# Kernel tuning notes

Hardware: AMD Instinct MI355X
Metric: run time of the kernel (lower is better)

## Reference

```python
import jax, jax.numpy as jnp
import numpy as np

B, S, D = 8, 2048, 128

def setup_inputs() -> dict:
    key = jax.random.key(0)
    kq, kk, kv, km = jax.random.split(key, 4)
    q = jax.random.normal(kq, (B, S, D), dtype=jnp.float32)
    k = jax.random.normal(kk, (B, S, D), dtype=jnp.float32)
    v = jax.random.normal(kv, (B, S, D), dtype=jnp.float32)
    mask = jax.random.randint(km, (B, S), 0, 2).astype(bool)  # True = masked out
    return {"q": q, "k": k, "v": v, "mask": mask}

def reference(q, k, v, mask):
    scaler = np.sqrt(D).astype(np.float32)
    # score[b, i, j] = <q_i, k_j> / sqrt(d_k)
    score = jnp.einsum('bik,bjk->bij', q, k) / scaler
    score = score - jnp.max(score, axis=-1, keepdims=True)
    e = jnp.exp(score)
    # mask is (B, S_kv): broadcast across query positions, zero out masked keys
    e = jnp.where(mask[:, None, :], 0.0, e)
    a = e / jnp.sum(e, axis=-1, keepdims=True)
    c = jnp.einsum('bij,bjd->bid', a, v)
    return c
```

## Files before the change

kernel.cpp:

```cpp
#include <hip/hip_runtime.h>
#include <hip/hip_fp16.h>
#include <math.h>

typedef __attribute__((ext_vector_type(8))) short short8;
typedef __attribute__((ext_vector_type(16))) float floatx16;
typedef __attribute__((ext_vector_type(2))) __bf16 bf16x2;

namespace {
constexpr int Bn = 8;
constexpr int Sn = 2048;
constexpr int Dn = 128;
constexpr int BQ = 128;
constexpr int BK = 64;
constexpr int QTILES = Sn / BQ;
constexpr int NKB = Sn / BK;
constexpr int ROWS = Bn * Sn;
constexpr int NSPLIT = 4;
constexpr float SC2 = 0.12753102063642597f;
constexpr int TILE_USH = BK * Dn;
}

#if __has_builtin(__builtin_amdgcn_exp2f)
#define EXP2(x) __builtin_amdgcn_exp2f(x)
#else
#define EXP2(x) exp2f(x)
#endif

__device__ __forceinline__ unsigned short f2bf(float x) {
  union { float f; unsigned u; } a; a.f = x;
  unsigned r = a.u + 0x7fffu + ((a.u >> 16) & 1u);
  return (unsigned short)(r >> 16);
}

__device__ __forceinline__ unsigned pack2bf(float x, float y) {
  union { bf16x2 b; unsigned u; } c;
  c.b[0] = (__bf16)x; c.b[1] = (__bf16)y;
  return c.u;
}

__device__ __forceinline__ void gl_lds16(const void* g, void* l, int lane) {
#if __has_builtin(__builtin_amdgcn_global_load_lds)
  (void)lane;
  __builtin_amdgcn_global_load_lds((const __attribute__((address_space(1))) unsigned int*)g,
                                   (__attribute__((address_space(3))) unsigned int*)l, 16, 0, 0);
#else
  *(float4*)((char*)l + lane * 16) = *(const float4*)g;
#endif
}

__global__ __launch_bounds__(256)
void prep(const float* __restrict__ kg, const float* __restrict__ vg,
          const unsigned char* __restrict__ mraw,
          unsigned short* __restrict__ Kpg, unsigned short* __restrict__ Vpg,
          float* __restrict__ mb2g) {
  __shared__ __align__(16) float Vf[16 * 136];
  const int p = blockIdx.x;
  const int b = p >> 7, q = p & 127;
  const int kb = q >> 2, k16 = q & 3;
  const int t = threadIdx.x;

  unsigned wv = ((const unsigned int*)mraw)[t];
  int any1  = __syncthreads_or((wv & 0x0000ff00u) ? 1 : 0);
  int any23 = __syncthreads_or((wv & 0xffff0000u) ? 1 : 0);
  const int mlayout = any1 ? 1 : (any23 ? 2 : 0);
  if (p < 64) {
    int idx = p * 256 + t;
    bool ms;
    if (mlayout == 1)      ms = mraw[idx] != 0;
    else if (mlayout == 2) ms = ((const float*)mraw)[idx] != 0.0f;
    else                   ms = ((const int*)mraw)[idx] != 0;
    mb2g[idx] = ms ? -1e30f : 0.0f;
  }

  const int j  = t >> 4;
  const int o8 = t & 15;
  const size_t base = ((size_t)(b * Sn + kb * 64 + k16 * 16 + j)) * 32 + o8 * 2;
  const float4* k4 = (const float4*)kg;
  const float4* v4 = (const float4*)vg;

  {
    float4 a = k4[base], bq = k4[base + 1];
    union { unsigned u[4]; short8 s8; } pk;
    pk.u[0] = pack2bf(a.x, a.y);   pk.u[1] = pack2bf(a.z, a.w);
    pk.u[2] = pack2bf(bq.x, bq.y); pk.u[3] = pack2bf(bq.z, bq.w);
    const int jl = k16 * 16 + j;
    *(short8*)(Kpg + (size_t)(b * NKB + kb) * TILE_USH + jl * 128 + ((o8 ^ (jl & 7)) * 8)) = pk.s8;
  }
  {
    float4 a = v4[base], bq = v4[base + 1];
    *(float4*)&Vf[j * 136 + o8 * 8]     = a;
    *(float4*)&Vf[j * 136 + o8 * 8 + 4] = bq;
  }
  __syncthreads();
  {
    const int d = t >> 1, h = t & 1;
    union { unsigned u[4]; short8 s8; } pv;
    #pragma unroll
    for (int i = 0; i < 4; ++i)
      pv.u[i] = pack2bf(Vf[(h * 8 + 2 * i) * 136 + d], Vf[(h * 8 + 2 * i + 1) * 136 + d]);
    const int og = k16 * 2 + h;
    *(short8*)(Vpg + (size_t)(b * NKB + kb) * TILE_USH + d * 64 + ((og ^ (d & 7)) * 8)) = pv.s8;
  }
}

template<int SPLIT, bool DIRECT>
__global__ __launch_bounds__(256, 2)
void attn_fwd(const float* __restrict__ qg,
              const unsigned short* __restrict__ Kpg,
              const unsigned short* __restrict__ Vpg,
              const float* __restrict__ mb2g,
              float* __restrict__ outg, __half* __restrict__ Op,
              float* __restrict__ Mp, float* __restrict__ Lp) {
  __shared__ __align__(16) unsigned short Khi[2][TILE_USH];
  __shared__ __align__(16) unsigned short Vt[2][TILE_USH];
  __shared__ __align__(16) unsigned short Pq[4 * 2048];

  const int tid = threadIdx.x;
  const int bid = blockIdx.x;
  const int b   = bid & 7;
  const int q0  = ((bid >> 3) & (QTILES - 1)) * BQ;
  const int s   = bid >> 7;
  const int kb0 = s * (NKB / SPLIT);
  const int kbN = kb0 + NKB / SPLIT;
  const int w   = tid >> 6;
  const int L   = tid & 63;
  const int q   = L & 31;
  const int h   = L >> 5;
  const int sw  = q & 7;

  const char* ktile = (const char*)(Kpg + (size_t)b * NKB * TILE_USH);
  const char* vtile = (const char*)(Vpg + (size_t)b * NKB * TILE_USH);
  const int stagebase = w * 4096;

  short8 qh[8], ql[8];
  {
    const float* qrow = qg + (size_t)(b * Sn + q0 + w * 32 + q) * Dn;
    #pragma unroll
    for (int kstep = 0; kstep < 8; ++kstep) {
      float4 f0 = *(const float4*)(qrow + kstep * 16 + h * 8);
      float4 f1 = *(const float4*)(qrow + kstep * 16 + h * 8 + 4);
      float xs[8] = {f0.x, f0.y, f0.z, f0.w, f1.x, f1.y, f1.z, f1.w};
      #pragma unroll
      for (int j = 0; j < 8; ++j) {
        unsigned short hi = f2bf(xs[j]);
        union { unsigned u; float f; } hv; hv.u = ((unsigned)hi) << 16;
        qh[kstep][j] = (short)hi;
        ql[kstep][j] = (short)f2bf(xs[j] - hv.f);
      }
    }
  }

  float m_i = -INFINITY, l_i = 0.0f;
  floatx16 O32[4];
  #pragma unroll
  for (int dg = 0; dg < 4; ++dg)
    #pragma unroll
    for (int r = 0; r < 16; ++r) O32[dg][r] = 0.0f;

  unsigned short* pwave = Pq + w * 2048;

  {
    const char* kt = ktile + (size_t)kb0 * (TILE_USH * 2);
    const char* vt = vtile + (size_t)kb0 * (TILE_USH * 2);
    #pragma unroll
    for (int i = 0; i < 4; ++i) {
      const int off = stagebase + i * 1024;
      gl_lds16(kt + off + L * 16, (char*)Khi[0] + off, L);
      gl_lds16(vt + off + L * 16, (char*)Vt[0] + off, L);
    }
  }

  for (int kb = kb0; kb < kbN; ++kb) {
    const int cur = (kb - kb0) & 1;
    __syncthreads();

    if (kb + 1 < kbN) {
      const char* kt = ktile + (size_t)(kb + 1) * (TILE_USH * 2);
      const char* vt = vtile + (size_t)(kb + 1) * (TILE_USH * 2);
      #pragma unroll
      for (int i = 0; i < 4; ++i) {
        const int off = stagebase + i * 1024;
        gl_lds16(kt + off + L * 16, (char*)Khi[cur ^ 1] + off, L);
        gl_lds16(vt + off + L * 16, (char*)Vt[cur ^ 1] + off, L);
      }
    }

    const unsigned short* Kc = Khi[cur];
    const unsigned short* Vc = Vt[cur];

    const float4* mb4 = (const float4*)(mb2g + b * Sn + kb * BK);
    float4 mbv[2][4];
    #pragma unroll
    for (int kg = 0; kg < 2; ++kg)
      #pragma unroll
      for (int ro = 0; ro < 4; ++ro) mbv[kg][ro] = mb4[kg * 8 + ro * 2 + h];

    floatx16 a32[2];
    #pragma unroll
    for (int kg = 0; kg < 2; ++kg)
      #pragma unroll
      for (int r = 0; r < 16; ++r) a32[kg][r] = 0.0f;
    #pragma unroll
    for (int kstep = 0; kstep < 8; ++kstep) {
      const int ko = ((kstep * 2 + h) ^ sw) * 8;
      #pragma unroll
      for (int kg = 0; kg < 2; ++kg) {
        short8 kf = *(const short8*)&Kc[(kg * 32 + q) * 128 + ko];
        a32[kg] = __builtin_amdgcn_mfma_f32_32x32x16_bf16(kf, qh[kstep], a32[kg], 0, 0, 0);
        a32[kg] = __builtin_amdgcn_mfma_f32_32x32x16_bf16(kf, ql[kstep], a32[kg], 0, 0, 0);
      }
    }

    #pragma unroll
    for (int kg = 0; kg < 2; ++kg)
      #pragma unroll
      for (int ro = 0; ro < 4; ++ro) {
        float4 f = mbv[kg][ro];
        a32[kg][4 * ro + 0] = fmaf(a32[kg][4 * ro + 0], SC2, f.x);
        a32[kg][4 * ro + 1] = fmaf(a32[kg][4 * ro + 1], SC2, f.y);
        a32[kg][4 * ro + 2] = fmaf(a32[kg][4 * ro + 2], SC2, f.z);
        a32[kg][4 * ro + 3] = fmaf(a32[kg][4 * ro + 3], SC2, f.w);
      }
    float mx = -INFINITY;
    #pragma unroll
    for (int kg = 0; kg < 2; ++kg)
      #pragma unroll
      for (int r = 0; r < 16; ++r) mx = fmaxf(mx, a32[kg][r]);
    mx = fmaxf(mx, __shfl_xor(mx, 32));
    const float mnew = fmaxf(m_i, mx);
    const float alpha = EXP2(m_i - mnew);
    float rs = 0.0f;
    #pragma unroll
    for (int kg = 0; kg < 2; ++kg)
      #pragma unroll
      for (int r = 0; r < 16; ++r) {
        float e = EXP2(a32[kg][r] - mnew);
        a32[kg][r] = e;
        rs += e;
      }
    rs += __shfl_xor(rs, 32);
    l_i = l_i * alpha + rs;
    m_i = mnew;

    #pragma unroll
    for (int kg = 0; kg < 2; ++kg)
      #pragma unroll
      for (int ro = 0; ro < 4; ++ro) {
        uint2 u;
        u.x = pack2bf(a32[kg][4 * ro + 0], a32[kg][4 * ro + 1]);
        u.y = pack2bf(a32[kg][4 * ro + 2], a32[kg][4 * ro + 3]);
        const int oct = kg * 4 + ro;
        *(uint2*)&pwave[q * 64 + ((oct ^ sw) * 8) + h * 4] = u;
      }

    if (!__all(alpha == 1.0f)) {
      #pragma unroll
      for (int dg = 0; dg < 4; ++dg)
        #pragma unroll
        for (int r = 0; r < 16; ++r) O32[dg][r] *= alpha;
    }

    #pragma unroll
    for (int k2 = 0; k2 < 4; ++k2) {
      const int ko = ((k2 * 2 + h) ^ sw) * 8;
      short8 pf = *(const short8*)&pwave[q * 64 + ko];
      #pragma unroll
      for (int dg = 0; dg < 4; ++dg) {
        short8 vf = *(const short8*)&Vc[(dg * 32 + q) * 64 + ko];
        O32[dg] = __builtin_amdgcn_mfma_f32_32x32x16_bf16(vf, pf, O32[dg], 0, 0, 0);
      }
    }
  }

  const int row = b * Sn + q0 + w * 32 + q;
  if constexpr (DIRECT) {
    const float inv = 1.0f / l_i;
    float* orow = outg + (size_t)row * Dn;
    #pragma unroll
    for (int dg = 0; dg < 4; ++dg)
      #pragma unroll
      for (int ro = 0; ro < 4; ++ro) {
        float4 f = make_float4(O32[dg][4 * ro] * inv,     O32[dg][4 * ro + 1] * inv,
                               O32[dg][4 * ro + 2] * inv, O32[dg][4 * ro + 3] * inv);
        *(float4*)&orow[dg * 32 + 8 * ro + 4 * h] = f;
      }
  } else {
    __half* orow = Op + ((size_t)s * ROWS + row) * Dn;
    #pragma unroll
    for (int dg = 0; dg < 4; ++dg)
      #pragma unroll
      for (int ro = 0; ro < 4; ++ro) {
        union { __half2 h2[2]; uint2 u; } pk;
        pk.h2[0] = __floats2half2_rn(O32[dg][4 * ro],     O32[dg][4 * ro + 1]);
        pk.h2[1] = __floats2half2_rn(O32[dg][4 * ro + 2], O32[dg][4 * ro + 3]);
        *(uint2*)&orow[dg * 32 + 8 * ro + 4 * h] = pk.u;
      }
    if (h == 0) {
      Mp[s * ROWS + row] = m_i;
      Lp[s * ROWS + row] = l_i;
    }
  }
}

__global__ __launch_bounds__(256)
void attn_combine(const __half* __restrict__ Op, const float* __restrict__ Mp,
                  const float* __restrict__ Lp, float4* __restrict__ out4) {
  const int gid = blockIdx.x * 256 + threadIdx.x;
  const int row = gid >> 5;
  const int c4  = gid & 31;
  float ms[NSPLIT];
  float m = -INFINITY;
  #pragma unroll
  for (int s = 0; s < NSPLIT; ++s) { ms[s] = Mp[s * ROWS + row]; m = fmaxf(m, ms[s]); }
  float l = 0.0f;
  float4 acc = make_float4(0.f, 0.f, 0.f, 0.f);
  #pragma unroll
  for (int s = 0; s < NSPLIT; ++s) {
    float wgt = EXP2(ms[s] - m);
    l = fmaf(Lp[s * ROWS + row], wgt, l);
    union { uint2 u; __half2 h2[2]; } pk;
    pk.u = ((const uint2*)Op)[(size_t)(s * ROWS + row) * 32 + c4];
    float2 f0 = __half22float2(pk.h2[0]);
    float2 f1 = __half22float2(pk.h2[1]);
    acc.x = fmaf(f0.x, wgt, acc.x);
    acc.y = fmaf(f0.y, wgt, acc.y);
    acc.z = fmaf(f1.x, wgt, acc.z);
    acc.w = fmaf(f1.y, wgt, acc.w);
  }
  float inv = 1.0f / l;
  out4[(size_t)row * 32 + c4] = make_float4(acc.x * inv, acc.y * inv, acc.z * inv, acc.w * inv);
}

extern "C" void kernel_launch(void* const* d_in, const int* in_sizes, int n_in,
                              void* d_out, int out_size, void* d_ws, size_t ws_size,
                              hipStream_t stream) {
  const float* q = (const float*)d_in[0];
  const float* k = (const float*)d_in[1];
  const float* v = (const float*)d_in[2];
  const unsigned char* m = (const unsigned char*)d_in[3];
  float* out = (float*)d_out;
  (void)in_sizes; (void)n_in; (void)out_size;

  constexpr size_t OPB = (size_t)NSPLIT * ROWS * Dn * sizeof(__half);
  constexpr size_t MLB = (size_t)NSPLIT * ROWS * sizeof(float);
  constexpr size_t KPB = (size_t)Bn * NKB * TILE_USH * 2;
  constexpr size_t MBB = (size_t)ROWS * sizeof(float);

  char* ws = (char*)d_ws;
  if (ws_size >= OPB + 2 * MLB + 2 * KPB + MBB) {
    __half* Op = (__half*)ws;
    float* Mp = (float*)(ws + OPB);
    float* Lp = (float*)(ws + OPB + MLB);
    unsigned short* Kp = (unsigned short*)(ws + OPB + 2 * MLB);
    unsigned short* Vp = (unsigned short*)(ws + OPB + 2 * MLB + KPB);
    float* mb2 = (float*)(ws + OPB + 2 * MLB + 2 * KPB);
    prep<<<dim3(Bn * NKB * 4), dim3(256), 0, stream>>>(k, v, m, Kp, Vp, mb2);
    attn_fwd<NSPLIT, false><<<dim3(Bn * QTILES * NSPLIT), dim3(256), 0, stream>>>(
        q, Kp, Vp, mb2, out, Op, Mp, Lp);
    attn_combine<<<dim3(ROWS * 32 / 256), dim3(256), 0, stream>>>(
        Op, Mp, Lp, (float4*)out);
  } else if (ws_size >= 2 * KPB + MBB) {
    unsigned short* Kp = (unsigned short*)ws;
    unsigned short* Vp = (unsigned short*)(ws + KPB);
    float* mb2 = (float*)(ws + 2 * KPB);
    prep<<<dim3(Bn * NKB * 4), dim3(256), 0, stream>>>(k, v, m, Kp, Vp, mb2);
    attn_fwd<1, true><<<dim3(Bn * QTILES), dim3(256), 0, stream>>>(
        q, Kp, Vp, mb2, out, nullptr, nullptr, nullptr);
  }
}
```

Baseline: 114.5 us.

## Keep P in registers via permlane swap, defer rescaling, prioritize MFMA

Removes the per-wave LDS round trip for the softmax probability tile. The packed bf16 P values are rearranged between lane halves with permlane32_swap, so the PV MFMA takes its operand straight from registers. Online-softmax rescaling of O and l is skipped unless the block max exceeds the running max by more than a threshold, with a final correction using the true max. The change also adds s_setprio around the MFMA sections and splits the max and sum reductions into multiple accumulators for ILP. The risk is fp16 overflow of unnormalized partial outputs when rescaling is deferred, and extra register pressure.

```diff
diff --git a/kernel.cpp b/kernel.cpp
--- a/kernel.cpp
+++ b/kernel.cpp
@@ -5,6 +5,7 @@
 typedef __attribute__((ext_vector_type(8))) short short8;
 typedef __attribute__((ext_vector_type(16))) float floatx16;
 typedef __attribute__((ext_vector_type(2))) __bf16 bf16x2;
+typedef __attribute__((ext_vector_type(2))) unsigned int uint2v;
 
 namespace {
 constexpr int Bn = 8;
@@ -17,6 +18,7 @@
 constexpr int ROWS = Bn * Sn;
 constexpr int NSPLIT = 4;
 constexpr float SC2 = 0.12753102063642597f;
+constexpr float DEFER_THR = 8.0f;
 constexpr int TILE_USH = BK * Dn;
 }
 
@@ -36,6 +38,20 @@
   union { bf16x2 b; unsigned u; } c;
   c.b[0] = (__bf16)x; c.b[1] = (__bf16)y;
   return c.u;
+}
+
+__device__ __forceinline__ uint2v pl32swap(unsigned a, unsigned b, int h) {
+#if __has_builtin(__builtin_amdgcn_permlane32_swap)
+  (void)h;
+  return __builtin_amdgcn_permlane32_swap(a, b, false, false);
+#else
+  unsigned ax = __shfl_xor((int)a, 32);
+  unsigned bx = __shfl_xor((int)b, 32);
+  uint2v r;
+  r[0] = h ? bx : a;
+  r[1] = h ? b : ax;
+  return r;
+#endif
 }
 
 __device__ __forceinline__ void gl_lds16(const void* g, void* l, int lane) {
@@ -113,7 +129,6 @@
               float* __restrict__ Mp, float* __restrict__ Lp) {
   __shared__ __align__(16) unsigned short Khi[2][TILE_USH];
   __shared__ __align__(16) unsigned short Vt[2][TILE_USH];
-  __shared__ __align__(16) unsigned short Pq[4 * 2048];
 
   const int tid = threadIdx.x;
   const int bid = blockIdx.x;
@@ -151,13 +166,12 @@
   }
 
   float m_i = -INFINITY, l_i = 0.0f;
+  float mtrue = -INFINITY;
   floatx16 O32[4];
   #pragma unroll
   for (int dg = 0; dg < 4; ++dg)
     #pragma unroll
     for (int r = 0; r < 16; ++r) O32[dg][r] = 0.0f;
-
-  unsigned short* pwave = Pq + w * 2048;
 
   {
     const char* kt = ktile + (size_t)kb0 * (TILE_USH * 2);
@@ -200,6 +214,7 @@
     for (int kg = 0; kg < 2; ++kg)
       #pragma unroll
       for (int r = 0; r < 16; ++r) a32[kg][r] = 0.0f;
+    __builtin_amdgcn_s_setprio(1);
     #pragma unroll
     for (int kstep = 0; kstep < 8; ++kstep) {
       const int ko = ((kstep * 2 + h) ^ sw) * 8;
@@ -210,6 +225,7 @@
         a32[kg] = __builtin_amdgcn_mfma_f32_32x32x16_bf16(kf, ql[kstep], a32[kg], 0, 0, 0);
       }
     }
+    __builtin_amdgcn_s_setprio(0);
 
     #pragma unroll
     for (int kg = 0; kg < 2; ++kg)
@@ -221,55 +237,76 @@
         a32[kg][4 * ro + 2] = fmaf(a32[kg][4 * ro + 2], SC2, f.z);
         a32[kg][4 * ro + 3] = fmaf(a32[kg][4 * ro + 3], SC2, f.w);
       }
-    float mx = -INFINITY;
-    #pragma unroll
-    for (int kg = 0; kg < 2; ++kg)
-      #pragma unroll
-      for (int r = 0; r < 16; ++r) mx = fmaxf(mx, a32[kg][r]);
+    float mxp[4] = {-INFINITY, -INFINITY, -INFINITY, -INFINITY};
+    #pragma unroll
+    for (int kg = 0; kg < 2; ++kg)
+      #pragma unroll
+      for (int r = 0; r < 16; ++r) mxp[r & 3] = fmaxf(mxp[r & 3], a32[kg][r]);
+    float mx = fmaxf(fmaxf(mxp[0], mxp[1]), fmaxf(mxp[2], mxp[3]));
     mx = fmaxf(mx, __shfl_xor(mx, 32));
-    const float mnew = fmaxf(m_i, mx);
-    const float alpha = EXP2(m_i - mnew);
-    float rs = 0.0f;
+    mtrue = fmaxf(mtrue, mx);
+
+    float mnew;
+    if (__all(mx <= m_i + DEFER_THR)) {
+      mnew = m_i;
+    } else {
+      mnew = fmaxf(m_i, mx);
+      const float alpha = EXP2(m_i - mnew);
+      l_i *= alpha;
+      #pragma unroll
+      for (int dg = 0; dg < 4; ++dg)
+        #pragma unroll
+        for (int r = 0; r < 16; ++r) O32[dg][r] *= alpha;
+    }
+
+    float rsp[4] = {0.f, 0.f, 0.f, 0.f};
     #pragma unroll
     for (int kg = 0; kg < 2; ++kg)
       #pragma unroll
       for (int r = 0; r < 16; ++r) {
         float e = EXP2(a32[kg][r] - mnew);
         a32[kg][r] = e;
-        rs += e;
-      }
+        rsp[r & 3] += e;
+      }
+    float rs = (rsp[0] + rsp[1]) + (rsp[2] + rsp[3]);
     rs += __shfl_xor(rs, 32);
-    l_i = l_i * alpha + rs;
+    l_i += rs;
     m_i = mnew;
 
-    #pragma unroll
-    for (int kg = 0; kg < 2; ++kg)
-      #pragma unroll
-      for (int ro = 0; ro < 4; ++ro) {
-        uint2 u;
-        u.x = pack2bf(a32[kg][4 * ro + 0], a32[kg][4 * ro + 1]);
-        u.y = pack2bf(a32[kg][4 * ro + 2], a32[kg][4 * ro + 3]);
-        const int oct = kg * 4 + ro;
-        *(uint2*)&pwave[q * 64 + ((oct ^ sw) * 8) + h * 4] = u;
-      }
-
-    if (!__all(alpha == 1.0f)) {
-      #pragma unroll
-      for (int dg = 0; dg < 4; ++dg)
+    unsigned xw[2][4][2];
+    #pragma unroll
+    for (int kg = 0; kg < 2; ++kg)
+      #pragma unroll
+      for (int m = 0; m < 4; ++m) {
+        xw[kg][m][0] = pack2bf(a32[kg][4 * m + 0], a32[kg][4 * m + 1]);
+        xw[kg][m][1] = pack2bf(a32[kg][4 * m + 2], a32[kg][4 * m + 3]);
+      }
+    unsigned pfw[4][4];
+    #pragma unroll
+    for (int kg = 0; kg < 2; ++kg)
+      #pragma unroll
+      for (int j = 0; j < 2; ++j)
         #pragma unroll
-        for (int r = 0; r < 16; ++r) O32[dg][r] *= alpha;
-    }
-
+        for (int c2 = 0; c2 < 2; ++c2) {
+          uint2v r = pl32swap(xw[kg][2 * j][c2], xw[kg][2 * j + 1][c2], h);
+          pfw[kg * 2 + j][c2]     = r[0];
+          pfw[kg * 2 + j][2 + c2] = r[1];
+        }
+
+    __builtin_amdgcn_s_setprio(1);
     #pragma unroll
     for (int k2 = 0; k2 < 4; ++k2) {
       const int ko = ((k2 * 2 + h) ^ sw) * 8;
-      short8 pf = *(const short8*)&pwave[q * 64 + ko];
+      union { unsigned u[4]; short8 s8; } pw;
+      pw.u[0] = pfw[k2][0]; pw.u[1] = pfw[k2][1];
+      pw.u[2] = pfw[k2][2]; pw.u[3] = pfw[k2][3];
       #pragma unroll
       for (int dg = 0; dg < 4; ++dg) {
         short8 vf = *(const short8*)&Vc[(dg * 32 + q) * 64 + ko];
-        O32[dg] = __builtin_amdgcn_mfma_f32_32x32x16_bf16(vf, pf, O32[dg], 0, 0, 0);
-      }
-    }
+        O32[dg] = __builtin_amdgcn_mfma_f32_32x32x16_bf16(vf, pw.s8, O32[dg], 0, 0, 0);
+      }
+    }
+    __builtin_amdgcn_s_setprio(0);
   }
 
   const int row = b * Sn + q0 + w * 32 + q;
@@ -285,19 +322,20 @@
         *(float4*)&orow[dg * 32 + 8 * ro + 4 * h] = f;
       }
   } else {
+    const float fin = EXP2(m_i - mtrue);
     __half* orow = Op + ((size_t)s * ROWS + row) * Dn;
     #pragma unroll
     for (int dg = 0; dg < 4; ++dg)
       #pragma unroll
       for (int ro = 0; ro < 4; ++ro) {
         union { __half2 h2[2]; uint2 u; } pk;
-        pk.h2[0] = __floats2half2_rn(O32[dg][4 * ro],     O32[dg][4 * ro + 1]);
-        pk.h2[1] = __floats2half2_rn(O32[dg][4 * ro + 2], O32[dg][4 * ro + 3]);
+        pk.h2[0] = __floats2half2_rn(O32[dg][4 * ro] * fin,     O32[dg][4 * ro + 1] * fin);
+        pk.h2[1] = __floats2half2_rn(O32[dg][4 * ro + 2] * fin, O32[dg][4 * ro + 3] * fin);
         *(uint2*)&orow[dg * 32 + 8 * ro + 4 * h] = pk.u;
       }
     if (h == 0) {
-      Mp[s * ROWS + row] = m_i;
-      Lp[s * ROWS + row] = l_i;
+      Mp[s * ROWS + row] = mtrue;
+      Lp[s * ROWS + row] = l_i * fin;
     }
   }
 }
```

Measured after the change: 115.4 us. Within noise of the previous version (+0.8%).
